# Performance work log

Measured on AMD Instinct MI355X. Metric: run time of the kernel, lower is better.

## Reference

```python
import jax, jax.numpy as jnp
import numpy as np
import math

IN_CH = 512
OUT_CH = 512
K = 3
STYLE_DIM = 512
RANK = 4
LORA_ALPHA_CONV = 1.0
LORA_ALPHA_FC = 1.0
CONV_SCALE = 1.0 / math.sqrt(IN_CH * K * K)   # 1/sqrt(fan_in)
MOD_SCALE = 1.0 / math.sqrt(STYLE_DIM)        # EqualLinear scale, lr_mul=1
EPS = 1e-8


def setup_inputs() -> dict:
    key = jax.random.key(0)
    ks = jax.random.split(key, 12)
    B, H, W = 8, 64, 64
    inp = {
        "input": jax.random.normal(ks[0], (B, IN_CH, H, W), dtype=jnp.float32),
        "style": jax.random.normal(ks[1], (B, STYLE_DIM), dtype=jnp.float32),
        # base conv weight [1, out, in, k, k]
        "weight": jax.random.normal(ks[2], (1, OUT_CH, IN_CH, K, K), dtype=jnp.float32),
        # LLoRAConv params (conv-weight LoRA)
        "ll_lora_B": jax.random.normal(ks[3], (OUT_CH, RANK), dtype=jnp.float32) / RANK ** (2.0 / 3.0),
        "ll_lora_B_inst": jax.random.normal(ks[4], (RANK, RANK, K * K), dtype=jnp.float32) * 0.1,
        "ll_lora_A": jax.random.normal(ks[5], (IN_CH, RANK), dtype=jnp.float32) / RANK ** (2.0 / 3.0),
        # CoLoREqualLinear (style modulation) params
        "mod_weight": jax.random.normal(ks[6], (IN_CH, STYLE_DIM), dtype=jnp.float32),
        "mod_bias": jnp.ones((IN_CH,), dtype=jnp.float32),  # bias_init=1
        # LoRAFC params on the modulation FC
        "fc_lora_A": jax.random.normal(ks[7], (STYLE_DIM, RANK), dtype=jnp.float32) / math.sqrt(RANK),
        "fc_lora_B": jax.random.normal(ks[8], (IN_CH, RANK), dtype=jnp.float32) * 0.1,
        "fc_lora_bias": jnp.ones((IN_CH,), dtype=jnp.float32),
    }
    return inp


def reference(input, style, weight, ll_lora_B, ll_lora_B_inst, ll_lora_A,
              mod_weight, mod_bias, fc_lora_A, fc_lora_B, fc_lora_bias):
    B, in_ch, H, W = input.shape
    out_ch = weight.shape[1]
    k = weight.shape[-1]
    pad = k // 2

    # --- LLoRAConv: LoRA-generated additive conv weight ---
    # torch: matmul([out,r], [r_batch, r, k2]) -> [r_batch, out, k2]
    Bm = jax.nn.relu(jnp.einsum('or,brk->bok', ll_lora_B, ll_lora_B_inst))
    # matmul([in,r_batch], [out, r_batch, k2]) -> [out, in, k2]
    w_add = jax.nn.relu(jnp.einsum('ib,bok->oik', ll_lora_A, Bm)) * LORA_ALPHA_CONV
    w5 = weight + w_add.reshape(1, out_ch, in_ch, k, k)  # [1, out, in, k, k]

    # --- CoLoREqualLinear with LoRAFC: style -> per-channel modulation ---
    w_fc = mod_weight + LORA_ALPHA_FC * (fc_lora_B @ fc_lora_A.T)  # [in, style_dim]
    b_fc = mod_bias + fc_lora_bias                                  # [in]
    s = style @ (w_fc * MOD_SCALE).T + b_fc                         # [B, in]

    # --- modulate / demodulate ---
    w = CONV_SCALE * w5 * s[:, None, :, None, None]                 # [B, out, in, k, k]
    demod = jax.lax.rsqrt(jnp.sum(w * w, axis=(2, 3, 4)) + EPS)     # [B, out]
    w = w * demod[:, :, None, None, None]

    # --- grouped conv: batch-as-groups ---
    wg = w.reshape(B * out_ch, in_ch, k, k)
    x = input.reshape(1, B * in_ch, H, W)
    out = jax.lax.conv_general_dilated(
        x, wg, window_strides=(1, 1), padding=((pad, pad), (pad, pad)),
        dimension_numbers=('NCHW', 'OIHW', 'NCHW'), feature_group_count=B)
    return out.reshape(B, out_ch, H, W)
```

## Files before the change

### kernel.cpp

```cpp
#include <hip/hip_runtime.h>
#include <hip/hip_bf16.h>
#include <math.h>

#define IC 512
#define OC 512
#define STYLE 512
#define BB 8
#define H_ 64
#define W_ 64
#define HW 4096
#define HP 66
#define KC 32
#define NCHUNK 16
#define USTRIDE 1056
#define ROWSTRIDE 4224
#define BUFSZ (6 * ROWSTRIDE)

typedef __attribute__((ext_vector_type(8))) __bf16 bf16x8;
typedef __attribute__((ext_vector_type(4))) float floatx4;

static __device__ __forceinline__ unsigned short f2bf(float f) {
    unsigned u = __builtin_bit_cast(unsigned, f);
    unsigned r = u + 0x7FFFu + ((u >> 16) & 1u);
    return (unsigned short)(r >> 16);
}

static __device__ __forceinline__ void gload_lds16(const unsigned short* g, unsigned char* l) {
    __builtin_amdgcn_global_load_lds((const __attribute__((address_space(1))) unsigned int*)g,
                                     (__attribute__((address_space(3))) unsigned int*)l,
                                     16, 0, 0);
}

__global__ void k_style(const float* __restrict__ style, const float* __restrict__ mod_weight,
                        const float* __restrict__ mod_bias, const float* __restrict__ fc_lora_A,
                        const float* __restrict__ fc_lora_B, const float* __restrict__ fc_lora_bias,
                        float* __restrict__ s_out) {
    int b = blockIdx.y;
    int i = blockIdx.x * 16 + (threadIdx.x >> 4);
    int jg = threadIdx.x & 15;
    float4 fb = *(const float4*)&fc_lora_B[i * 4];
    const float* st = style + b * STYLE;
    const float* mw = mod_weight + (size_t)i * STYLE;
    float acc = 0.f;
    for (int j = jg * 32; j < jg * 32 + 32; ++j) {
        float4 fa = *(const float4*)&fc_lora_A[j * 4];
        float w = mw[j] + fb.x * fa.x + fb.y * fa.y + fb.z * fa.z + fb.w * fa.w;
        acc += st[j] * w;
    }
    #pragma unroll
    for (int off = 8; off; off >>= 1) acc += __shfl_down(acc, off, 16);
    if (jg == 0) {
        float mod_scale = 1.0f / sqrtf((float)STYLE);
        s_out[b * IC + i] = mod_scale * acc + mod_bias[i] + fc_lora_bias[i];
    }
}

__global__ void k_weight(const float* __restrict__ weight, const float* __restrict__ llB,
                         const float* __restrict__ llBinst, const float* __restrict__ llA,
                         unsigned short* __restrict__ wb, float* __restrict__ W2) {
    int gid = blockIdx.x * 256 + threadIdx.x;
    int o = gid >> 9, i = gid & 511;
    float4 vB = *(const float4*)&llB[o * 4];
    float4 vA = *(const float4*)&llA[i * 4];
    const float* wrow = weight + (size_t)(o * IC + i) * 9;
    int lane = ((i >> 3) & 3) * 16 + (o & 15);
    size_t wbase = (((size_t)((o >> 6) * 4 + ((o >> 4) & 3)) * 16 + (i >> 5)) * 64 + lane) * 8 + (i & 7);
    float w2 = 0.f;
    #pragma unroll
    for (int k = 0; k < 9; ++k) {
        float wadd = 0.f;
        #pragma unroll
        for (int bb = 0; bb < 4; ++bb) {
            float bm = vB.x * llBinst[(bb * 4 + 0) * 9 + k] + vB.y * llBinst[(bb * 4 + 1) * 9 + k]
                     + vB.z * llBinst[(bb * 4 + 2) * 9 + k] + vB.w * llBinst[(bb * 4 + 3) * 9 + k];
            bm = fmaxf(bm, 0.f);
            float a = (bb == 0) ? vA.x : (bb == 1) ? vA.y : (bb == 2) ? vA.z : vA.w;
            wadd += a * bm;
        }
        wadd = fmaxf(wadd, 0.f);
        float w5 = wrow[k] + wadd;
        wb[(size_t)k * 262144 + wbase] = f2bf(w5);
        w2 += w5 * w5;
    }
    W2[gid] = w2;
}

__global__ void k_scale(const float* __restrict__ W2, const float* __restrict__ s,
                        float* __restrict__ scale) {
    int b = blockIdx.y;
    int o = blockIdx.x * 16 + (threadIdx.x >> 4);
    int jg = threadIdx.x & 15;
    const float* w2r = W2 + (size_t)o * IC;
    const float* sr = s + b * IC;
    float acc = 0.f;
    for (int i = jg * 32; i < jg * 32 + 32; ++i) { float sv = sr[i]; acc += w2r[i] * sv * sv; }
    #pragma unroll
    for (int off = 8; off; off >>= 1) acc += __shfl_down(acc, off, 16);
    if (jg == 0) {
        float cs = 1.0f / sqrtf((float)(IC * 9));
        scale[b * OC + o] = cs * rsqrtf(cs * cs * acc + 1e-8f);
    }
}

__global__ void k_stage_x(const float* __restrict__ x, const float* __restrict__ s,
                          unsigned short* __restrict__ xm) {
    __shared__ float tile[128 * 65];
    int cc = blockIdx.x;
    int hp = blockIdx.y;
    int b  = blockIdx.z;
    int c0 = cc * 128;
    int tid = threadIdx.x;
    if (hp == 0 || hp == HP - 1) {
        unsigned short* dst = xm + (size_t)(b * HP + hp) * 32768 + cc * 8192;
        uint4 z = make_uint4(0, 0, 0, 0);
        #pragma unroll
        for (int p = 0; p < 4; ++p)
            *(uint4*)(dst + (size_t)(p * 256 + tid) * 8) = z;
        return;
    }
    int h = hp - 1;
    const float* xin = x + (((size_t)b * IC + c0) * H_ + h) * W_;
    #pragma unroll
    for (int p = 0; p < 32; ++p) {
        int idx = p * 256 + tid;
        int c = idx >> 6, w = idx & 63;
        tile[c * 65 + w] = xin[(size_t)c * HW + w];
    }
    __syncthreads();
    const float* sb = s + b * IC + c0;
    #pragma unroll
    for (int p = 0; p < 4; ++p) {
        int idx = p * 256 + tid;
        int cil = idx >> 8;
        int u   = (idx >> 6) & 3;
        int w   = idx & 63;
        int cb  = cil * 32 + u * 8;
        unsigned int packed[4];
        #pragma unroll
        for (int k = 0; k < 4; ++k) {
            unsigned lo = f2bf(tile[(cb + 2 * k) * 65 + w] * sb[cb + 2 * k]);
            unsigned hi = f2bf(tile[(cb + 2 * k + 1) * 65 + w] * sb[cb + 2 * k + 1]);
            packed[k] = lo | (hi << 16);
        }
        size_t g = (((size_t)(b * HP + hp) * 16 + (cc * 4 + cil)) * 4 + u) * 64 + w;
        *(uint4*)(xm + g * 8) = make_uint4(packed[0], packed[1], packed[2], packed[3]);
    }
}

__global__ __launch_bounds__(256, 3) void k_conv(const unsigned short* __restrict__ wb,
                                                 const unsigned short* __restrict__ xm,
                                                 const float* __restrict__ scale,
                                                 float* __restrict__ out) {
    __shared__ unsigned char xs[2 * BUFSZ];
    const int tid = threadIdx.x;
    const int wave = tid >> 6, lane = tid & 63;
    const int l16 = lane & 15, lq = lane >> 4;
    const int wgid = blockIdx.x;
    const int ot = wgid & 7;
    const int r  = wgid >> 3;
    const int ht = r & 15;
    const int b  = r >> 4;
    const int om = ot * 64;
    const int h0 = ht * 4;

    if (tid < 96) {
        int bsel = tid >= 48;
        int t48 = tid - bsel * 48;
        int row = t48 >> 3;
        int rem = t48 & 7;
        int u = rem >> 1;
        int side = rem & 1;
        uint4 z = make_uint4(0, 0, 0, 0);
        *(uint4*)(xs + bsel * BUFSZ + row * ROWSTRIDE + u * USTRIDE + side * 65 * 16) = z;
    }

    floatx4 acc[4][4];
    #pragma unroll
    for (int mt = 0; mt < 4; ++mt)
        #pragma unroll
        for (int nt = 0; nt < 4; ++nt)
            acc[mt][nt] = (floatx4){0.f, 0.f, 0.f, 0.f};

    const unsigned short* xmb = xm + (size_t)b * HP * 32768;
    const unsigned short* wlb = wb + (size_t)ot * 32768 + (size_t)lane * 8;

    #pragma unroll
    for (int j = 0; j < 6; ++j)
        gload_lds16(xmb + ((((size_t)(h0 + j) * 16 + 0) * 4 + wave) * 64 + lane) * 8,
                    xs + (size_t)j * ROWSTRIDE + wave * USTRIDE + 16);

    int cur = 0;
    for (int ci = 0; ci < NCHUNK; ++ci) {
        __syncthreads();
        if (ci + 1 < NCHUNK) {
            #pragma unroll
            for (int j = 0; j < 6; ++j)
                gload_lds16(xmb + ((((size_t)(h0 + j) * 16 + (ci + 1)) * 4 + wave) * 64 + lane) * 8,
                            xs + (size_t)(cur ^ 1) * BUFSZ + (size_t)j * ROWSTRIDE + wave * USTRIDE + 16);
        }
        const unsigned char* buf = xs + (size_t)cur * BUFSZ;
        const unsigned short* wlc = wlb + (size_t)ci * 512;
        #pragma unroll
        for (int kh = 0; kh < 3; ++kh) {
            #pragma unroll
            for (int dw = 0; dw < 3; ++dw) {
                const int t = kh * 3 + dw;
                bf16x8 af[4], bv[4];
                #pragma unroll
                for (int mt = 0; mt < 4; ++mt)
                    af[mt] = *(const bf16x8*)(wlc + (size_t)t * 262144 + mt * 8192);
                #pragma unroll
                for (int nt = 0; nt < 4; ++nt)
                    bv[nt] = *(const bf16x8*)(buf + (size_t)(wave + kh) * ROWSTRIDE + lq * USTRIDE
                                              + (nt * 16 + l16 + dw) * 16);
                #pragma unroll
                for (int mt = 0; mt < 4; ++mt)
                    #pragma unroll
                    for (int nt = 0; nt < 4; ++nt)
                        acc[mt][nt] = __builtin_amdgcn_mfma_f32_16x16x32_bf16(af[mt], bv[nt], acc[mt][nt], 0, 0, 0);
            }
        }
        cur ^= 1;
    }

    __syncthreads();
    float* ebuf = (float*)xs + wave * 1088;
    const int h = h0 + wave;
    const float* scb = scale + b * OC + om;
    #pragma unroll
    for (int mt = 0; mt < 4; ++mt) {
        float4 sc = *(const float4*)&scb[mt * 16 + lq * 4];
        const float* scp = (const float*)&sc;
        #pragma unroll
        for (int nt = 0; nt < 4; ++nt)
            #pragma unroll
            for (int r2 = 0; r2 < 4; ++r2)
                ebuf[(lq * 4 + r2) * 68 + nt * 16 + l16] = acc[mt][nt][r2] * scp[r2];
        __syncthreads();
        #pragma unroll
        for (int q = 0; q < 4; ++q) {
            int r0 = q * 4 + (lane >> 4);
            int c0 = (lane & 15) * 4;
            float4 v = *(float4*)&ebuf[r0 * 68 + c0];
            *(float4*)&out[((size_t)(b * OC + om + mt * 16 + r0)) * HW + h * W_ + c0] = v;
        }
        __syncthreads();
    }
}

extern "C" void kernel_launch(void* const* d_in, const int* in_sizes, int n_in,
                              void* d_out, int out_size, void* d_ws, size_t ws_size,
                              hipStream_t stream) {
    const float* input   = (const float*)d_in[0];
    const float* style   = (const float*)d_in[1];
    const float* weight  = (const float*)d_in[2];
    const float* llB     = (const float*)d_in[3];
    const float* llBinst = (const float*)d_in[4];
    const float* llA     = (const float*)d_in[5];
    const float* mod_w   = (const float*)d_in[6];
    const float* mod_b   = (const float*)d_in[7];
    const float* fcA     = (const float*)d_in[8];
    const float* fcB     = (const float*)d_in[9];
    const float* fcBias  = (const float*)d_in[10];
    float* out = (float*)d_out;

    char* ws = (char*)d_ws;
    float* s_ws            = (float*)(ws + 0);
    float* scale_ws        = (float*)(ws + 16384);
    float* W2_ws           = (float*)(ws + 32768);
    unsigned short* wb_ws  = (unsigned short*)(ws + 32768 + 1048576);
    unsigned short* xm_ws  = (unsigned short*)(ws + 32768 + 1048576 + 4718592);

    k_style<<<dim3(32, 8), 256, 0, stream>>>(style, mod_w, mod_b, fcA, fcB, fcBias, s_ws);
    k_weight<<<1024, 256, 0, stream>>>(weight, llB, llBinst, llA, wb_ws, W2_ws);
    k_scale<<<dim3(32, 8), 256, 0, stream>>>(W2_ws, s_ws, scale_ws);
    k_stage_x<<<dim3(4, 66, 8), 256, 0, stream>>>(input, s_ws, xm_ws);
    k_conv<<<1024, 256, 0, stream>>>(wb_ws, xm_ws, scale_ws, out);
}
```

Measured before the change: 331.9 us.

## Enlarge conv tile to 16 rows per block with two rows per wave

Each conv workgroup now covers 16 output rows using 8 waves, and each wave computes two rows, so every weight fragment feeds twice as many MFMAs. The input halo overhead shrinks from 6 staged rows per 4 output rows to 18 per 16. In exchange the block uses about 152KB of LDS, doubles the accumulator registers, and the grid drops to 256 blocks, which could hurt occupancy and load balance across CUs.

```diff
diff --git a/kernel.cpp b/kernel.cpp
--- a/kernel.cpp
+++ b/kernel.cpp
@@ -14,7 +14,8 @@
 #define NCHUNK 16
 #define USTRIDE 1056
 #define ROWSTRIDE 4224
-#define BUFSZ (6 * ROWSTRIDE)
+#define XROWS 18
+#define BUFX (XROWS * ROWSTRIDE)
 
 typedef __attribute__((ext_vector_type(8))) __bf16 bf16x8;
 typedef __attribute__((ext_vector_type(4))) float floatx4;
@@ -147,77 +148,91 @@
     }
 }
 
-__global__ __launch_bounds__(256, 3) void k_conv(const unsigned short* __restrict__ wb,
+__global__ __launch_bounds__(512, 2) void k_conv(const unsigned short* __restrict__ wb,
                                                  const unsigned short* __restrict__ xm,
                                                  const float* __restrict__ scale,
                                                  float* __restrict__ out) {
-    __shared__ unsigned char xs[2 * BUFSZ];
+    __shared__ unsigned char xs[2 * BUFX];
     const int tid = threadIdx.x;
     const int wave = tid >> 6, lane = tid & 63;
     const int l16 = lane & 15, lq = lane >> 4;
     const int wgid = blockIdx.x;
     const int ot = wgid & 7;
     const int r  = wgid >> 3;
-    const int ht = r & 15;
-    const int b  = r >> 4;
+    const int ht = r & 3;
+    const int b  = r >> 2;
     const int om = ot * 64;
-    const int h0 = ht * 4;
-
-    if (tid < 96) {
-        int bsel = tid >= 48;
-        int t48 = tid - bsel * 48;
-        int row = t48 >> 3;
-        int rem = t48 & 7;
+    const int h0 = ht * 16;
+    const int r0 = wave * 2;
+
+    if (tid < 288) {
+        int bsel = tid >= 144;
+        int t144 = tid - bsel * 144;
+        int row = t144 >> 3;
+        int rem = t144 & 7;
         int u = rem >> 1;
         int side = rem & 1;
         uint4 z = make_uint4(0, 0, 0, 0);
-        *(uint4*)(xs + bsel * BUFSZ + row * ROWSTRIDE + u * USTRIDE + side * 65 * 16) = z;
-    }
-
-    floatx4 acc[4][4];
-    #pragma unroll
-    for (int mt = 0; mt < 4; ++mt)
-        #pragma unroll
-        for (int nt = 0; nt < 4; ++nt)
-            acc[mt][nt] = (floatx4){0.f, 0.f, 0.f, 0.f};
+        *(uint4*)(xs + (size_t)bsel * BUFX + (size_t)row * ROWSTRIDE + u * USTRIDE + side * 65 * 16) = z;
+    }
+
+    floatx4 acc[2][4][4];
+    #pragma unroll
+    for (int rr = 0; rr < 2; ++rr)
+        #pragma unroll
+        for (int mt = 0; mt < 4; ++mt)
+            #pragma unroll
+            for (int nt = 0; nt < 4; ++nt)
+                acc[rr][mt][nt] = (floatx4){0.f, 0.f, 0.f, 0.f};
 
     const unsigned short* xmb = xm + (size_t)b * HP * 32768;
     const unsigned short* wlb = wb + (size_t)ot * 32768 + (size_t)lane * 8;
 
     #pragma unroll
-    for (int j = 0; j < 6; ++j)
-        gload_lds16(xmb + ((((size_t)(h0 + j) * 16 + 0) * 4 + wave) * 64 + lane) * 8,
-                    xs + (size_t)j * ROWSTRIDE + wave * USTRIDE + 16);
+    for (int j = 0; j < 9; ++j) {
+        const int g = wave * 9 + j;
+        const int row = g >> 2, u = g & 3;
+        gload_lds16(xmb + ((((size_t)(h0 + row) * 16 + 0) * 4 + u) * 64 + lane) * 8,
+                    xs + (size_t)row * ROWSTRIDE + u * USTRIDE + 16);
+    }
 
     int cur = 0;
     for (int ci = 0; ci < NCHUNK; ++ci) {
         __syncthreads();
         if (ci + 1 < NCHUNK) {
             #pragma unroll
-            for (int j = 0; j < 6; ++j)
-                gload_lds16(xmb + ((((size_t)(h0 + j) * 16 + (ci + 1)) * 4 + wave) * 64 + lane) * 8,
-                            xs + (size_t)(cur ^ 1) * BUFSZ + (size_t)j * ROWSTRIDE + wave * USTRIDE + 16);
-        }
-        const unsigned char* buf = xs + (size_t)cur * BUFSZ;
+            for (int j = 0; j < 9; ++j) {
+                const int g = wave * 9 + j;
+                const int row = g >> 2, u = g & 3;
+                gload_lds16(xmb + ((((size_t)(h0 + row) * 16 + (ci + 1)) * 4 + u) * 64 + lane) * 8,
+                            xs + (size_t)(cur ^ 1) * BUFX + (size_t)row * ROWSTRIDE + u * USTRIDE + 16);
+            }
+        }
+        const unsigned char* buf = xs + (size_t)cur * BUFX;
         const unsigned short* wlc = wlb + (size_t)ci * 512;
         #pragma unroll
         for (int kh = 0; kh < 3; ++kh) {
             #pragma unroll
             for (int dw = 0; dw < 3; ++dw) {
                 const int t = kh * 3 + dw;
-                bf16x8 af[4], bv[4];
+                bf16x8 af[4], bva[4], bvb[4];
                 #pragma unroll
                 for (int mt = 0; mt < 4; ++mt)
                     af[mt] = *(const bf16x8*)(wlc + (size_t)t * 262144 + mt * 8192);
                 #pragma unroll
-                for (int nt = 0; nt < 4; ++nt)
-                    bv[nt] = *(const bf16x8*)(buf + (size_t)(wave + kh) * ROWSTRIDE + lq * USTRIDE
-                                              + (nt * 16 + l16 + dw) * 16);
+                for (int nt = 0; nt < 4; ++nt) {
+                    bva[nt] = *(const bf16x8*)(buf + (size_t)(r0 + kh) * ROWSTRIDE + lq * USTRIDE
+                                               + (nt * 16 + l16 + dw) * 16);
+                    bvb[nt] = *(const bf16x8*)(buf + (size_t)(r0 + 1 + kh) * ROWSTRIDE + lq * USTRIDE
+                                               + (nt * 16 + l16 + dw) * 16);
+                }
                 #pragma unroll
                 for (int mt = 0; mt < 4; ++mt)
                     #pragma unroll
-                    for (int nt = 0; nt < 4; ++nt)
-                        acc[mt][nt] = __builtin_amdgcn_mfma_f32_16x16x32_bf16(af[mt], bv[nt], acc[mt][nt], 0, 0, 0);
+                    for (int nt = 0; nt < 4; ++nt) {
+                        acc[0][mt][nt] = __builtin_amdgcn_mfma_f32_16x16x32_bf16(af[mt], bva[nt], acc[0][mt][nt], 0, 0, 0);
+                        acc[1][mt][nt] = __builtin_amdgcn_mfma_f32_16x16x32_bf16(af[mt], bvb[nt], acc[1][mt][nt], 0, 0, 0);
+                    }
             }
         }
         cur ^= 1;
@@ -225,26 +240,29 @@
 
     __syncthreads();
     float* ebuf = (float*)xs + wave * 1088;
-    const int h = h0 + wave;
     const float* scb = scale + b * OC + om;
     #pragma unroll
-    for (int mt = 0; mt < 4; ++mt) {
-        float4 sc = *(const float4*)&scb[mt * 16 + lq * 4];
-        const float* scp = (const float*)&sc;
-        #pragma unroll
-        for (int nt = 0; nt < 4; ++nt)
-            #pragma unroll
-            for (int r2 = 0; r2 < 4; ++r2)
-                ebuf[(lq * 4 + r2) * 68 + nt * 16 + l16] = acc[mt][nt][r2] * scp[r2];
-        __syncthreads();
-        #pragma unroll
-        for (int q = 0; q < 4; ++q) {
-            int r0 = q * 4 + (lane >> 4);
-            int c0 = (lane & 15) * 4;
-            float4 v = *(float4*)&ebuf[r0 * 68 + c0];
-            *(float4*)&out[((size_t)(b * OC + om + mt * 16 + r0)) * HW + h * W_ + c0] = v;
-        }
-        __syncthreads();
+    for (int rr = 0; rr < 2; ++rr) {
+        const int h = h0 + r0 + rr;
+        #pragma unroll
+        for (int mt = 0; mt < 4; ++mt) {
+            float4 sc = *(const float4*)&scb[mt * 16 + lq * 4];
+            const float* scp = (const float*)&sc;
+            #pragma unroll
+            for (int nt = 0; nt < 4; ++nt)
+                #pragma unroll
+                for (int r2 = 0; r2 < 4; ++r2)
+                    ebuf[(lq * 4 + r2) * 68 + nt * 16 + l16] = acc[rr][mt][nt][r2] * scp[r2];
+            __syncthreads();
+            #pragma unroll
+            for (int q = 0; q < 4; ++q) {
+                int rq = q * 4 + (lane >> 4);
+                int c0 = (lane & 15) * 4;
+                float4 v = *(float4*)&ebuf[rq * 68 + c0];
+                *(float4*)&out[((size_t)(b * OC + om + mt * 16 + rq)) * HW + h * W_ + c0] = v;
+            }
+            __syncthreads();
+        }
     }
 }
 
@@ -275,5 +293,5 @@
     k_weight<<<1024, 256, 0, stream>>>(weight, llB, llBinst, llA, wb_ws, W2_ws);
     k_scale<<<dim3(32, 8), 256, 0, stream>>>(W2_ws, s_ws, scale_ws);
     k_stage_x<<<dim3(4, 66, 8), 256, 0, stream>>>(input, s_ws, xm_ws);
-    k_conv<<<1024, 256, 0, stream>>>(wb_ws, xm_ws, scale_ws, out);
-}
+    k_conv<<<256, 512, 0, stream>>>(wb_ws, xm_ws, scale_ws, out);
+}
```

Measured after the change: 342.7 us. +3.3%, slower.

## Share staged input tile across two output-channel tiles with 512-thread blocks

Applied to the files above, without the earlier changes.

Conv blocks now have 8 waves covering two 64-channel output tiles over the same 4-row spatial tile, so each staged LDS input chunk is reused by twice as many waves. Grid is halved and each wave stages 3 of the 24 row/u slices instead of 6. This halves global input reads and LDS staging traffic per output, at the cost of larger blocks, more waves per barrier, and tighter register/occupancy limits under launch_bounds(512,4).

```diff
diff --git a/kernel.cpp b/kernel.cpp
--- a/kernel.cpp
+++ b/kernel.cpp
@@ -147,7 +147,16 @@
     }
 }
 
-__global__ __launch_bounds__(256, 3) void k_conv(const unsigned short* __restrict__ wb,
+#define STAGE(CN, BSEL)                                                                          \
+    _Pragma("unroll")                                                                            \
+    for (int j = 0; j < 3; ++j) {                                                                \
+        const int g_ = wave * 3 + j;                                                             \
+        const int row_ = g_ >> 2, u_ = g_ & 3;                                                   \
+        gload_lds16(xmb + ((((size_t)(h0 + row_) * 16 + (CN)) * 4 + u_) * 64 + lane) * 8,        \
+                    xs + (size_t)(BSEL) * BUFSZ + (size_t)row_ * ROWSTRIDE + u_ * USTRIDE + 16); \
+    }
+
+__global__ __launch_bounds__(512, 4) void k_conv(const unsigned short* __restrict__ wb,
                                                  const unsigned short* __restrict__ xm,
                                                  const float* __restrict__ scale,
                                                  float* __restrict__ out) {
@@ -155,11 +164,14 @@
     const int tid = threadIdx.x;
     const int wave = tid >> 6, lane = tid & 63;
     const int l16 = lane & 15, lq = lane >> 4;
+    const int ow = wave >> 2;
+    const int wr = wave & 3;
     const int wgid = blockIdx.x;
-    const int ot = wgid & 7;
-    const int r  = wgid >> 3;
-    const int ht = r & 15;
-    const int b  = r >> 4;
+    const int ot2 = wgid & 3;
+    const int rr = wgid >> 2;
+    const int ht = rr & 15;
+    const int b  = rr >> 4;
+    const int ot = ot2 * 2 + ow;
     const int om = ot * 64;
     const int h0 = ht * 4;
 
@@ -184,20 +196,12 @@
     const unsigned short* xmb = xm + (size_t)b * HP * 32768;
     const unsigned short* wlb = wb + (size_t)ot * 32768 + (size_t)lane * 8;
 
-    #pragma unroll
-    for (int j = 0; j < 6; ++j)
-        gload_lds16(xmb + ((((size_t)(h0 + j) * 16 + 0) * 4 + wave) * 64 + lane) * 8,
-                    xs + (size_t)j * ROWSTRIDE + wave * USTRIDE + 16);
+    STAGE(0, 0)
 
     int cur = 0;
     for (int ci = 0; ci < NCHUNK; ++ci) {
         __syncthreads();
-        if (ci + 1 < NCHUNK) {
-            #pragma unroll
-            for (int j = 0; j < 6; ++j)
-                gload_lds16(xmb + ((((size_t)(h0 + j) * 16 + (ci + 1)) * 4 + wave) * 64 + lane) * 8,
-                            xs + (size_t)(cur ^ 1) * BUFSZ + (size_t)j * ROWSTRIDE + wave * USTRIDE + 16);
-        }
+        if (ci + 1 < NCHUNK) STAGE(ci + 1, cur ^ 1)
         const unsigned char* buf = xs + (size_t)cur * BUFSZ;
         const unsigned short* wlc = wlb + (size_t)ci * 512;
         #pragma unroll
@@ -211,7 +215,7 @@
                     af[mt] = *(const bf16x8*)(wlc + (size_t)t * 262144 + mt * 8192);
                 #pragma unroll
                 for (int nt = 0; nt < 4; ++nt)
-                    bv[nt] = *(const bf16x8*)(buf + (size_t)(wave + kh) * ROWSTRIDE + lq * USTRIDE
+                    bv[nt] = *(const bf16x8*)(buf + (size_t)(wr + kh) * ROWSTRIDE + lq * USTRIDE
                                               + (nt * 16 + l16 + dw) * 16);
                 #pragma unroll
                 for (int mt = 0; mt < 4; ++mt)
@@ -225,7 +229,7 @@
 
     __syncthreads();
     float* ebuf = (float*)xs + wave * 1088;
-    const int h = h0 + wave;
+    const int h = h0 + wr;
     const float* scb = scale + b * OC + om;
     #pragma unroll
     for (int mt = 0; mt < 4; ++mt) {
@@ -275,5 +279,5 @@
     k_weight<<<1024, 256, 0, stream>>>(weight, llB, llBinst, llA, wb_ws, W2_ws);
     k_scale<<<dim3(32, 8), 256, 0, stream>>>(W2_ws, s_ws, scale_ws);
     k_stage_x<<<dim3(4, 66, 8), 256, 0, stream>>>(input, s_ws, xm_ws);
-    k_conv<<<1024, 256, 0, stream>>>(wb_ws, xm_ws, scale_ws, out);
-}
+    k_conv<<<512, 512, 0, stream>>>(wb_ws, xm_ws, scale_ws, out);
+}
```

New measurement: 321.9 us. -3.0%, faster.
